# Kernel optimization log

Hardware: AMD Instinct MI355X
Metric: run time of the kernel (lower is better)

Reference implementation:

```python
import jax, jax.numpy as jnp
import numpy as np
import math

B, T, D, H = 4, 2048, 1024, 16
HD = D // H  # 64

def setup_inputs() -> dict:
    key = jax.random.key(0)
    ks = jax.random.split(key, 11)
    s = 1.0 / math.sqrt(D)
    return {
        "q": jax.random.normal(ks[0], (B, T, D), jnp.float32),
        "k": jax.random.normal(ks[1], (B, T, D), jnp.float32),
        "v": jax.random.normal(ks[2], (B, T, D), jnp.float32),
        "Wq": jax.random.normal(ks[3], (D, D), jnp.float32) * s,
        "bq": jnp.zeros((D,), jnp.float32),
        "Wk": jax.random.normal(ks[4], (D, D), jnp.float32) * s,
        "bk": jnp.zeros((D,), jnp.float32),
        "Wv": jax.random.normal(ks[5], (D, D), jnp.float32) * s,
        "bv": jnp.zeros((D,), jnp.float32),
        "Wo": jax.random.normal(ks[6], (D, D), jnp.float32) * s,
        "bo": jnp.zeros((D,), jnp.float32),
    }

def reference(q, k, v, Wq, bq, Wk, bk, Wv, bv, Wo, bo):
    # Linear projections (torch Linear: x @ W.T + b)
    qp = q @ Wq.T + bq
    kp = k @ Wk.T + bk
    vp = v @ Wv.T + bv
    # [B, T, D] -> [B, H, T, HD]
    def split(x):
        return x.reshape(B, T, H, HD).transpose(0, 2, 1, 3)
    qh, kh, vh = split(qp), split(kp), split(vp)
    # scaled dot-product attention
    score = jnp.einsum('bhqd,bhkd->bhqk', qh, kh) / math.sqrt(HD)
    attn = jax.nn.softmax(score, axis=-1)
    out = jnp.einsum('bhqk,bhkd->bhqd', attn, vh)
    # merge heads and output projection
    out = out.transpose(0, 2, 1, 3).reshape(B, T, D)
    return out @ Wo.T + bo
```

## Files before the change

kernel.cpp:

```cpp
#include <hip/hip_runtime.h>
#include <hip/hip_bf16.h>
#include <stdint.h>

#define B_ 4
#define T_ 2048
#define D_ 1024
#define H_ 16
#define HD_ 64
#define NKT (T_ / 64)

typedef __bf16 bf16;
typedef __bf16 bf16x8 __attribute__((ext_vector_type(8)));
typedef __bf16 bf16x4 __attribute__((ext_vector_type(4)));
typedef float f32x4 __attribute__((ext_vector_type(4)));
typedef uint32_t u32x4 __attribute__((ext_vector_type(4)));

#define QSCALE 0.18033688011112042f

__device__ __forceinline__ float fast_exp2(float x) {
#if __has_builtin(__builtin_amdgcn_exp2f)
    return __builtin_amdgcn_exp2f(x);
#else
    return exp2f(x);
#endif
}

__device__ __forceinline__ void async_load16(const bf16* g, const bf16* lds_uniform) {
    __builtin_amdgcn_global_load_lds(
        (const __attribute__((address_space(1))) uint32_t*)(uintptr_t)g,
        (__attribute__((address_space(3))) uint32_t*)(uintptr_t)lds_uniform,
        16, 0, 0);
}

__device__ __forceinline__ uint32_t pack2_bf16(float lo, float hi) {
    union { uint32_t u; __bf16 h[2]; } r;
    r.h[0] = (__bf16)lo;
    r.h[1] = (__bf16)hi;
    return r.u;
}

__device__ __forceinline__ void permswap16(uint32_t& a, uint32_t& b) {
    asm("v_permlane16_swap_b32 %0, %1" : "+v"(a), "+v"(b));
}

__global__ __launch_bounds__(256) void cast_all(const float* __restrict__ q, bf16* __restrict__ dq,
                                                const float* __restrict__ k, bf16* __restrict__ dk,
                                                const float* __restrict__ v, bf16* __restrict__ dv,
                                                const float* __restrict__ w0, bf16* __restrict__ e0,
                                                const float* __restrict__ w1, bf16* __restrict__ e1,
                                                const float* __restrict__ w2, bf16* __restrict__ e2,
                                                const float* __restrict__ w3, bf16* __restrict__ e3) {
    long i = blockIdx.x * 256 + threadIdx.x;
    const float* s;
    bf16* d;
    if (blockIdx.y < 3) {
        s = blockIdx.y == 0 ? q : (blockIdx.y == 1 ? k : v);
        d = blockIdx.y == 0 ? dq : (blockIdx.y == 1 ? dk : dv);
    } else {
        const long per = (long)(D_ * D_) / 4;
        long wsel = i / per;
        if (wsel >= 4) return;
        i -= wsel * per;
        s = wsel == 0 ? w0 : (wsel == 1 ? w1 : (wsel == 2 ? w2 : w3));
        d = wsel == 0 ? e0 : (wsel == 1 ? e1 : (wsel == 2 ? e2 : e3));
    }
    f32x4 val = ((const f32x4*)s)[i];
    bf16x4 o;
    o.x = (bf16)val.x; o.y = (bf16)val.y; o.z = (bf16)val.z; o.w = (bf16)val.w;
    ((bf16x4*)d)[i] = o;
}

template <typename OutT, int VMODE>
__device__ __forceinline__ void gemm_body(const bf16* __restrict__ A,
                                          const bf16* __restrict__ W,
                                          const float* __restrict__ bias,
                                          OutT* __restrict__ C,
                                          int lin, float scale,
                                          bf16* As, bf16* Bs, bf16* Tt) {
    const int K = D_, N = D_;
    const int tid = threadIdx.x;
    const int wid = tid >> 6, lane = tid & 63;
    const int quad = lane >> 4, l15 = lane & 15;
    const int wm = (wid >> 1) * 64, wn = (wid & 1) * 64;
    const int bx = N >> 7;
    const int ty = (lin & 7) + 8 * (lin / (8 * bx));
    const int tx = (lin >> 3) % bx;
    const long rowA0 = (long)ty * 128;
    const long rowB0 = (long)tx * 128;
    const int srow = lane >> 2;
    const int schunk = (lane & 3) * 8;
    const int sbase = (wid * 32) * 32;

    f32x4 acc[4][4];
#pragma unroll
    for (int i = 0; i < 4; i++)
#pragma unroll
        for (int j = 0; j < 4; j++) acc[i][j] = (f32x4){0.f, 0.f, 0.f, 0.f};

#pragma unroll
    for (int s = 0; s < 2; s++) {
        int r = wid * 32 + s * 16 + srow;
        async_load16(&A[(rowA0 + r) * K + schunk], &As[sbase + s * 16 * 32]);
        async_load16(&W[(rowB0 + r) * K + schunk], &Bs[sbase + s * 16 * 32]);
    }
    __syncthreads();

    const int NIT = K >> 5;
    for (int it = 0; it < NIT; it++) {
        const int cur = it & 1;
        const int co = cur * (128 * 32);
        if (it + 1 < NIT) {
            const int k1 = (it + 1) << 5;
            const int no = (cur ^ 1) * (128 * 32);
#pragma unroll
            for (int s = 0; s < 2; s++) {
                int r = wid * 32 + s * 16 + srow;
                async_load16(&A[(rowA0 + r) * K + k1 + schunk], &As[no + sbase + s * 16 * 32]);
                async_load16(&W[(rowB0 + r) * K + k1 + schunk], &Bs[no + sbase + s * 16 * 32]);
            }
        }
        bf16x8 af[4], bfr[4];
#pragma unroll
        for (int i = 0; i < 4; i++)
            af[i] = *(const bf16x8*)&As[co + (wm + i * 16 + l15) * 32 + quad * 8];
#pragma unroll
        for (int j = 0; j < 4; j++)
            bfr[j] = *(const bf16x8*)&Bs[co + (wn + j * 16 + l15) * 32 + quad * 8];
#pragma unroll
        for (int i = 0; i < 4; i++)
#pragma unroll
            for (int j = 0; j < 4; j++)
                acc[i][j] = __builtin_amdgcn_mfma_f32_16x16x32_bf16(af[i], bfr[j],
                                                                    acc[i][j], 0, 0, 0);
        __syncthreads();
    }

    if constexpr (VMODE == 0) {
#pragma unroll
        for (int i = 0; i < 4; i++) {
            long m = rowA0 + wm + i * 16 + quad * 4;
#pragma unroll
            for (int j = 0; j < 4; j++) {
                long n = rowB0 + wn + j * 16 + l15;
                float bb = bias[n];
#pragma unroll
                for (int r = 0; r < 4; r++) {
                    float v = (acc[i][j][r] + bb) * scale;
                    C[(m + r) * N + n] = (OutT)v;
                }
            }
        }
    } else {
        const long bidx = rowA0 >> 11;
        const int t0 = (int)(rowA0 & 2047);
#pragma unroll
        for (int p2 = 0; p2 < 2; p2++) {
            if (p2) __syncthreads();
#pragma unroll
            for (int j2 = 0; j2 < 2; j2++) {
                int j = p2 * 2 + j2;
                int nl = wn + j * 16 + l15;
                int rr = (nl & 31) + ((nl >> 6) << 5);
                float bb = bias[rowB0 + nl];
#pragma unroll
                for (int i = 0; i < 4; i++) {
                    int ml = wm + i * 16 + quad * 4;
                    bf16x4 ov = {(bf16)(acc[i][j][0] + bb), (bf16)(acc[i][j][1] + bb),
                                 (bf16)(acc[i][j][2] + bb), (bf16)(acc[i][j][3] + bb)};
                    *(bf16x4*)&Tt[rr * 136 + ml] = ov;
                }
            }
            __syncthreads();
#pragma unroll
            for (int p = 0; p < 4; p++) {
                int idx = p * 16 + (tid >> 4);
                int c = tid & 15;
                bf16x8 val = *(const bf16x8*)&Tt[idx * 136 + c * 8];
                int n = (int)rowB0 + (idx & 31) + p2 * 32 + ((idx >> 5) << 6);
                long vrow = (bidx * H_ + (n >> 6)) * (long)HD_ + (n & 63);
                int cp = (c & ~3) | ((c & 1) << 1) | ((c & 2) >> 1);
                *(bf16x8*)&((bf16*)C)[vrow * T_ + t0 + cp * 8] = val;
            }
        }
    }
}

__global__ __launch_bounds__(256) void gemm_qkv(const bf16* __restrict__ Xq,
                                                const bf16* __restrict__ WqB,
                                                const float* __restrict__ bq,
                                                bf16* __restrict__ Qp,
                                                const bf16* __restrict__ Xk,
                                                const bf16* __restrict__ WkB,
                                                const float* __restrict__ bk,
                                                bf16* __restrict__ Kp,
                                                const bf16* __restrict__ Xv,
                                                const bf16* __restrict__ WvB,
                                                const float* __restrict__ bv,
                                                bf16* __restrict__ VtG) {
    __shared__ __align__(16) char sm[32768];
    bf16* As = (bf16*)sm;
    bf16* Bs = (bf16*)(sm + 16384);
    bf16* Tt = (bf16*)sm;
    const int p = blockIdx.x >> 9;
    const int lin = blockIdx.x & 511;
    if (p == 0)
        gemm_body<bf16, 0>(Xq, WqB, bq, Qp, lin, QSCALE, As, Bs, Tt);
    else if (p == 1)
        gemm_body<bf16, 0>(Xk, WkB, bk, Kp, lin, 1.f, As, Bs, Tt);
    else
        gemm_body<bf16, 1>(Xv, WvB, bv, VtG, lin, 1.f, As, Bs, Tt);
}

__global__ __launch_bounds__(256) void gemm_out(const bf16* __restrict__ Op,
                                                const bf16* __restrict__ WoB,
                                                const float* __restrict__ bo,
                                                float* __restrict__ out) {
    __shared__ __align__(16) char sm[32768];
    bf16* As = (bf16*)sm;
    bf16* Bs = (bf16*)(sm + 16384);
    gemm_body<float, 0>(Op, WoB, bo, out, blockIdx.x, 1.f, As, Bs, nullptr);
}

__global__ __launch_bounds__(512, 8) void attn_kernel(const bf16* __restrict__ Qp,
                                                      const bf16* __restrict__ Kp,
                                                      const bf16* __restrict__ VT,
                                                      bf16* __restrict__ Op) {
    __shared__ bf16 smem[4][64 * 64];
    const int tid = threadIdx.x;
    const int wid = tid >> 6, lane = tid & 63;
    const int quad = lane >> 4, l15 = lane & 15;
    const int q7 = l15 & 7;
    const int lin = blockIdx.x;
    const int bh = (lin & 7) + 8 * (lin >> 7);
    const int qt = (lin >> 3) & 15;
    const int b = bh >> 4, h = bh & 15;
    const long tok0 = (long)b * T_ + (long)qt * 128 + wid * 16;
    const int hcol = h * HD_;
    const long vrow0 = ((long)bh) * HD_;
    const int g_sw = ((lane & 7) ^ (lane >> 3)) * 8;
    const int srow = lane >> 3;
    const int sbase = (wid * 8) * 64;

    {
        const long krow0 = (long)b * T_;
        const int r = wid * 8 + srow;
        async_load16(&Kp[(krow0 + r) * D_ + hcol + g_sw], &smem[0][sbase]);
        async_load16(&VT[(vrow0 + r) * T_ + g_sw], &smem[2][sbase]);
    }

    bf16x8 bq0 = *(const bf16x8*)&Qp[(tok0 + l15) * D_ + hcol + quad * 8];
    bf16x8 bq1 = *(const bf16x8*)&Qp[(tok0 + l15) * D_ + hcol + 32 + quad * 8];

    const u32x4 onesu = {0x3F803F80u, 0x3F803F80u, 0x3F803F80u, 0x3F803F80u};
    const bf16x8 ones = __builtin_bit_cast(bf16x8, onesu);
    const f32x4 z4 = (f32x4){0.f, 0.f, 0.f, 0.f};

    const int pat0 = (quad ^ q7) * 8;
    const int pat1 = ((4 + quad) ^ q7) * 8;

    f32x4 o[4];
#pragma unroll
    for (int mt = 0; mt < 4; mt++) o[mt] = (f32x4){0.f, 0.f, 0.f, 0.f};
    f32x4 ls = z4;

    __syncthreads();

    const int h0 = wid & 1;

    for (int kt = 0; kt < NKT; kt++) {
        const int cur = kt & 1;
        if (kt + 1 < NKT) {
            const long krow1 = (long)b * T_ + (long)(kt + 1) * 64;
            const int nb = cur ^ 1;
            const int r = wid * 8 + srow;
            async_load16(&Kp[(krow1 + r) * D_ + hcol + g_sw], &smem[nb][sbase]);
            async_load16(&VT[(vrow0 + r) * T_ + (long)(kt + 1) * 64 + g_sw],
                         &smem[2 + nb][sbase]);
        }
        const bf16* Ksc = smem[cur];
        const bf16* Vsc = smem[2 + cur];

        auto half_step = [&](int hh) {
            uint32_t pA[2], pB[2];
#pragma unroll
            for (int mt = 0; mt < 2; mt++) {
                const bf16* kr = &Ksc[(hh * 32 + mt * 16 + l15) * 64];
                bf16x8 ak0 = *(const bf16x8*)&kr[pat0];
                bf16x8 ak1 = *(const bf16x8*)&kr[pat1];
                f32x4 s = __builtin_amdgcn_mfma_f32_16x16x32_bf16(ak0, bq0, z4, 0, 0, 0);
                s = __builtin_amdgcn_mfma_f32_16x16x32_bf16(ak1, bq1, s, 0, 0, 0);
                float p0 = fast_exp2(s[0]), p1 = fast_exp2(s[1]);
                float p2 = fast_exp2(s[2]), p3 = fast_exp2(s[3]);
                pA[mt] = pack2_bf16(p0, p1);
                pB[mt] = pack2_bf16(p2, p3);
            }
            permswap16(pA[0], pA[1]);
            permswap16(pB[0], pB[1]);
            u32x4 f = {pA[0], pB[0], pA[1], pB[1]};
            bf16x8 pb = __builtin_bit_cast(bf16x8, f);
            ls = __builtin_amdgcn_mfma_f32_16x16x32_bf16(ones, pb, ls, 0, 0, 0);
            const int vch = hh ? pat1 : pat0;
#pragma unroll
            for (int mt = 0; mt < 4; mt++) {
                bf16x8 av = *(const bf16x8*)&Vsc[(mt * 16 + l15) * 64 + vch];
                o[mt] = __builtin_amdgcn_mfma_f32_16x16x32_bf16(av, pb, o[mt], 0, 0, 0);
            }
        };
        half_step(h0);
        half_step(h0 ^ 1);
        __syncthreads();
    }

    const float linv = 1.f / ls[0];

    bf16* ew = (bf16*)smem + wid * (16 * 64);
#pragma unroll
    for (int mt = 0; mt < 4; mt++) {
        bf16x4 ov = {(bf16)(o[mt][0] * linv), (bf16)(o[mt][1] * linv),
                     (bf16)(o[mt][2] * linv), (bf16)(o[mt][3] * linv)};
        *(bf16x4*)&ew[l15 * 64 + (((mt * 2 + (quad >> 1)) ^ q7) * 8) + (quad & 1) * 4] = ov;
    }
#pragma unroll
    for (int p2 = 0; p2 < 2; p2++) {
        int q = p2 * 8 + (lane >> 3);
        int dc = lane & 7;
        bf16x8 ov = *(const bf16x8*)&ew[q * 64 + ((dc ^ (q & 7)) * 8)];
        *(bf16x8*)&Op[(tok0 + q) * D_ + hcol + dc * 8] = ov;
    }
}

extern "C" void kernel_launch(void* const* d_in, const int* in_sizes, int n_in,
                              void* d_out, int out_size, void* d_ws, size_t ws_size,
                              hipStream_t stream) {
    const float* q  = (const float*)d_in[0];
    const float* k  = (const float*)d_in[1];
    const float* v  = (const float*)d_in[2];
    const float* Wq = (const float*)d_in[3];
    const float* bq = (const float*)d_in[4];
    const float* Wk = (const float*)d_in[5];
    const float* bk = (const float*)d_in[6];
    const float* Wv = (const float*)d_in[7];
    const float* bv = (const float*)d_in[8];
    const float* Wo = (const float*)d_in[9];
    const float* bo = (const float*)d_in[10];
    float* out = (float*)d_out;

    const size_t MD = (size_t)B_ * T_ * D_;
    const size_t DD = (size_t)D_ * D_;
    char* ws = (char*)d_ws;
    bf16* Xq  = (bf16*)ws; ws += MD * 2;
    bf16* Xk  = (bf16*)ws; ws += MD * 2;
    bf16* Xv  = (bf16*)ws; ws += MD * 2;
    bf16* WqB = (bf16*)ws; ws += DD * 2;
    bf16* WkB = (bf16*)ws; ws += DD * 2;
    bf16* WvB = (bf16*)ws; ws += DD * 2;
    bf16* WoB = (bf16*)ws; ws += DD * 2;
    bf16* Qp  = (bf16*)ws; ws += MD * 2;
    bf16* Kp  = (bf16*)ws; ws += MD * 2;
    bf16* VtG = (bf16*)ws; ws += MD * 2;
    bf16* Op  = (bf16*)ws; ws += MD * 2;

    cast_all<<<dim3(MD / 4 / 256, 4), 256, 0, stream>>>(q, Xq, k, Xk, v, Xv,
                                                        Wq, WqB, Wk, WkB, Wv, WvB, Wo, WoB);

    gemm_qkv<<<3 * 512, 256, 0, stream>>>(Xq, WqB, bq, Qp, Xk, WkB, bk, Kp, Xv, WvB, bv, VtG);

    attn_kernel<<<B_ * H_ * (T_ / 128), 512, 0, stream>>>(Qp, Kp, VtG, Op);

    gemm_out<<<512, 256, 0, stream>>>(Op, WoB, bo, out);
}
```

Measured before the change: 331.5 us.

## Rewrite output projection GEMM with 64x128 tiles and double-buffered async loads

Replaces the shared gemm_body call in the output projection with a dedicated kernel that uses 64x128 tiles and K-steps of 32, double-buffering A and W tiles in shared memory through async loads. The grid grows from 512 to 1024 blocks, giving more parallelism across CUs for the M=8192, N=1024 GEMM. The kernel also uses a remapped block index for L2 locality. Smaller tiles mean less reuse per load and more synchronisation steps, and the fp32 output stores are written per element without vectorisation.

```diff
diff --git a/kernel.cpp b/kernel.cpp
--- a/kernel.cpp
+++ b/kernel.cpp
@@ -211,14 +211,82 @@
         gemm_body<bf16, 1>(Xv, WvB, bv, VtG, lin, 1.f, As, Bs, Tt);
 }
 
-__global__ __launch_bounds__(256) void gemm_out(const bf16* __restrict__ Op,
-                                                const bf16* __restrict__ WoB,
-                                                const float* __restrict__ bo,
+__global__ __launch_bounds__(256) void gemm_out(const bf16* __restrict__ A,
+                                                const bf16* __restrict__ W,
+                                                const float* __restrict__ bias,
                                                 float* __restrict__ out) {
-    __shared__ __align__(16) char sm[32768];
-    bf16* As = (bf16*)sm;
-    bf16* Bs = (bf16*)(sm + 16384);
-    gemm_body<float, 0>(Op, WoB, bo, out, blockIdx.x, 1.f, As, Bs, nullptr);
+    __shared__ __align__(16) bf16 As[2][64 * 32];
+    __shared__ __align__(16) bf16 Bs[2][128 * 32];
+    const int K = D_, N = D_;
+    const int tid = threadIdx.x;
+    const int wid = tid >> 6, lane = tid & 63;
+    const int quad = lane >> 4, l15 = lane & 15;
+    const int wm = (wid >> 1) * 32, wn = (wid & 1) * 64;
+    const int lin = blockIdx.x;
+    const int ty = (lin & 7) + 8 * (lin >> 6);
+    const int tx = (lin >> 3) & 7;
+    const long rowA0 = (long)ty * 64;
+    const long rowB0 = (long)tx * 128;
+    const int srow = lane >> 2;
+    const int schunk = (lane & 3) * 8;
+    const int abase = (wid * 16) * 32;
+    const int bbase = (wid * 32) * 32;
+
+    f32x4 acc[2][4];
+#pragma unroll
+    for (int i = 0; i < 2; i++)
+#pragma unroll
+        for (int j = 0; j < 4; j++) acc[i][j] = (f32x4){0.f, 0.f, 0.f, 0.f};
+
+    async_load16(&A[(rowA0 + wid * 16 + srow) * K + schunk], &As[0][abase]);
+#pragma unroll
+    for (int s = 0; s < 2; s++) {
+        int r = wid * 32 + s * 16 + srow;
+        async_load16(&W[(rowB0 + r) * K + schunk], &Bs[0][bbase + s * 16 * 32]);
+    }
+    __syncthreads();
+
+    const int NIT = K >> 5;
+    for (int it = 0; it < NIT; it++) {
+        const int cur = it & 1;
+        if (it + 1 < NIT) {
+            const int k1 = (it + 1) << 5;
+            const int nb = cur ^ 1;
+            async_load16(&A[(rowA0 + wid * 16 + srow) * K + k1 + schunk], &As[nb][abase]);
+#pragma unroll
+            for (int s = 0; s < 2; s++) {
+                int r = wid * 32 + s * 16 + srow;
+                async_load16(&W[(rowB0 + r) * K + k1 + schunk], &Bs[nb][bbase + s * 16 * 32]);
+            }
+        }
+        bf16x8 af[2], bfr[4];
+#pragma unroll
+        for (int i = 0; i < 2; i++)
+            af[i] = *(const bf16x8*)&As[cur][(wm + i * 16 + l15) * 32 + quad * 8];
+#pragma unroll
+        for (int j = 0; j < 4; j++)
+            bfr[j] = *(const bf16x8*)&Bs[cur][(wn + j * 16 + l15) * 32 + quad * 8];
+#pragma unroll
+        for (int i = 0; i < 2; i++)
+#pragma unroll
+            for (int j = 0; j < 4; j++)
+                acc[i][j] = __builtin_amdgcn_mfma_f32_16x16x32_bf16(af[i], bfr[j],
+                                                                    acc[i][j], 0, 0, 0);
+        __syncthreads();
+    }
+
+#pragma unroll
+    for (int i = 0; i < 2; i++) {
+        long m = rowA0 + wm + i * 16 + quad * 4;
+#pragma unroll
+        for (int j = 0; j < 4; j++) {
+            long n = rowB0 + wn + j * 16 + l15;
+            float bb = bias[n];
+#pragma unroll
+            for (int r = 0; r < 4; r++)
+                out[(m + r) * N + n] = acc[i][j][r] + bb;
+        }
+    }
 }
 
 __global__ __launch_bounds__(512, 8) void attn_kernel(const bf16* __restrict__ Qp,
@@ -367,5 +435,5 @@
 
     attn_kernel<<<B_ * H_ * (T_ / 128), 512, 0, stream>>>(Qp, Kp, VtG, Op);
 
-    gemm_out<<<512, 256, 0, stream>>>(Op, WoB, bo, out);
-}
+    gemm_out<<<(B_ * T_ / 64) * (D_ / 128), 256, 0, stream>>>(Op, WoB, bo, out);
+}
```

Measured after the change: 343.7 us. +3.7%, slower.
